# Kernel optimization log

Measured on AMD Instinct MI355X. Metric: run time of the kernel, lower is better.

## Reference

```python
import jax, jax.numpy as jnp
import numpy as np

K = 11
EPS = 1e-6


def _box_sum(a):
    # a: [B, H, W] -> KxK zero-padded local sum (equivalent to nn.Unfold padding=K//2 then sum)
    return jax.lax.reduce_window(a, 0.0, jax.lax.add,
                                 window_dimensions=(1, K, K),
                                 window_strides=(1, 1, 1),
                                 padding='SAME')


def setup_inputs() -> dict:
    key = jax.random.key(0)
    k1, k2 = jax.random.split(key)
    x = jax.random.normal(k1, (8, 3, 1024, 1024), dtype=jnp.float32)
    y = jax.random.normal(k2, (8, 3, 1024, 1024), dtype=jnp.float32)
    return {"x": x, "y": y}


def reference(x, y):
    # Channel-reduce first, then local KxK box sums (math-identical to the
    # unfold-based sum over (C, K, K) with zero padding).
    xx = _box_sum((x * x).sum(axis=1))   # [B, H, W]
    yy = _box_sum((y * y).sum(axis=1))
    xy = _box_sum((x * y).sum(axis=1))
    x_norm = jnp.sqrt(xx)
    y_norm = jnp.sqrt(yy)
    return xy / (x_norm * y_norm + EPS)
```

## Files before the change

### kernel.cpp

```cpp
#include <hip/hip_runtime.h>
#include <math.h>

#define NB 8
#define NC 3
#define NH 1024
#define NW 1024
#define EPS 1e-6f

#define BAND 128
#define CH 32
#define KSTEPS (CH + 10)
#define PADW 144

__global__ __launch_bounds__(64, 2)
void lcs_kernel(const float* __restrict__ x, const float* __restrict__ y,
                float* __restrict__ out) {
    __shared__ __align__(16) float P[2][3][PADW];

    const int l   = threadIdx.x;
    const int bid = blockIdx.x;
    const int b     = bid >> 8;
    const int rem   = bid & 255;
    const int band0 = (rem & 7) * BAND;
    const int r0    = (rem >> 3) * CH;

    const size_t chan = (size_t)NH * NW;
    const float* xb = x + (size_t)b * NC * chan;
    const float* yb = y + (size_t)b * NC * chan;

    const int gc0 = band0 - 8 + 2 * l;
    const int gcE = band0 + 120 + 2 * l;
    const float mm = (gc0 >= 0) ? 1.f : 0.f;
    const float me = (l < 8 && gcE + 1 <= NW - 1) ? 1.f : 0.f;
    const int o0 = (gc0 >= 0) ? gc0 : 0;
    const int oE = (me > 0.f) ? gcE : 0;

    float2 cur[12], nx1[12], nx2[12];
    auto ldrow = [&](int gr, float2* d) {
        const int rc = gr < 0 ? 0 : (gr > NH - 1 ? NH - 1 : gr);
        const size_t ro = (size_t)rc * NW;
        #pragma unroll
        for (int c = 0; c < 3; ++c) {
            const float* xr = xb + c * chan + ro;
            const float* yr = yb + c * chan + ro;
            d[c]     = *(const float2*)(xr + o0);
            d[3 + c] = *(const float2*)(yr + o0);
            d[6 + c] = *(const float2*)(xr + oE);
            d[9 + c] = *(const float2*)(yr + oE);
        }
    };

    ldrow(r0 - 5, cur);
    ldrow(r0 - 4, nx1);

    float2 ring[3][11];
    #pragma unroll
    for (int p = 0; p < 3; ++p)
        #pragma unroll
        for (int s = 0; s < 11; ++s) ring[p][s] = make_float2(0.f, 0.f);
    float2 vs[3] = {make_float2(0.f,0.f), make_float2(0.f,0.f), make_float2(0.f,0.f)};

    for (int g = 0; g < 4; ++g) {
        const int gg = g & 1;
        #pragma unroll
        for (int s = 0; s < 11; ++s) {
            const int k = g * 11 + s;
            if (k >= KSTEPS) continue;

            if (k + 2 < KSTEPS) ldrow(r0 - 3 + k, nx2);

            float2 pxx = make_float2(0.f,0.f), pyy = pxx, pxy = pxx;
            float2 qxx = pxx, qyy = pxx, qxy = pxx;
            #pragma unroll
            for (int c = 0; c < 3; ++c) {
                const float2 xm = cur[c],   ym = cur[3+c];
                const float2 xe = cur[6+c], ye = cur[9+c];
                pxx.x += xm.x*xm.x; pxx.y += xm.y*xm.y;
                pyy.x += ym.x*ym.x; pyy.y += ym.y*ym.y;
                pxy.x += xm.x*ym.x; pxy.y += xm.y*ym.y;
                qxx.x += xe.x*xe.x; qxx.y += xe.y*xe.y;
                qyy.x += ye.x*ye.x; qyy.y += ye.y*ye.y;
                qxy.x += xe.x*ye.x; qxy.y += xe.y*ye.y;
            }
            const int gr = r0 - 5 + k;
            const float rmf = (gr >= 0 && gr < NH) ? 1.f : 0.f;
            const float cmM = rmf * mm, cmE = rmf * me;
            pxx.x *= cmM; pxx.y *= cmM; pyy.x *= cmM; pyy.y *= cmM;
            pxy.x *= cmM; pxy.y *= cmM;
            qxx.x *= cmE; qxx.y *= cmE; qyy.x *= cmE; qyy.y *= cmE;
            qxy.x *= cmE; qxy.y *= cmE;

            const int pp = gg ^ (s & 1);
            float* Pb = &P[pp][0][0];

            ((float2*)(Pb + 0*PADW))[l] = pxx;
            ((float2*)(Pb + 1*PADW))[l] = pyy;
            ((float2*)(Pb + 2*PADW))[l] = pxy;
            if (l < 8) {
                ((float2*)(Pb + 0*PADW))[64 + l] = qxx;
                ((float2*)(Pb + 1*PADW))[64 + l] = qyy;
                ((float2*)(Pb + 2*PADW))[64 + l] = qxy;
            }
            __builtin_amdgcn_wave_barrier();

            #pragma unroll
            for (int p = 0; p < 3; ++p) {
                const float* Pq = Pb + p * PADW;
                float2 t[7];
                #pragma unroll
                for (int j = 0; j < 7; ++j)
                    t[j] = *(const float2*)(Pq + 2*l + 2 + 2*j);
                float h0 = ((t[0].y + t[1].x) + (t[1].y + t[2].x))
                         + ((t[2].y + t[3].x) + (t[3].y + t[4].x))
                         + ((t[4].y + t[5].x) + t[5].y);
                float h1 = h0 - t[0].y + t[6].x;
                vs[p].x += h0 - ring[p][s].x;
                vs[p].y += h1 - ring[p][s].y;
                ring[p][s].x = h0;
                ring[p][s].y = h1;
            }

            if (k >= 10) {
                const int orow = r0 + k - 10;
                const float d0 = __builtin_amdgcn_sqrtf(vs[0].x) *
                                 __builtin_amdgcn_sqrtf(vs[1].x) + EPS;
                const float d1 = __builtin_amdgcn_sqrtf(vs[0].y) *
                                 __builtin_amdgcn_sqrtf(vs[1].y) + EPS;
                float2 o;
                o.x = vs[2].x * __builtin_amdgcn_rcpf(d0);
                o.y = vs[2].y * __builtin_amdgcn_rcpf(d1);
                *(float2*)(out + ((size_t)b * NH + orow) * NW + band0 + 2*l) = o;
            }

            if (k + 1 < KSTEPS) {
                #pragma unroll
                for (int i = 0; i < 12; ++i) { cur[i] = nx1[i]; nx1[i] = nx2[i]; }
            }
        }
    }
}

extern "C" void kernel_launch(void* const* d_in, const int* in_sizes, int n_in,
                              void* d_out, int out_size, void* d_ws, size_t ws_size,
                              hipStream_t stream) {
    const float* x = (const float*)d_in[0];
    const float* y = (const float*)d_in[1];
    float* out = (float*)d_out;
    lcs_kernel<<<dim3(2048), dim3(64), 0, stream>>>(x, y, out);
}
```

Before: 241.3 us.

## Stream input rows into LDS via global_load_lds triple buffer

Replaces the register-held triple-buffered row prefetch with direct global-to-LDS loads (16-byte per lane) into a rotating three-slot LDS buffer, synchronized with explicit s_waitcnt vmcnt counts. Each lane loads one contiguous 16-byte segment per channel instead of two scattered float2 loads, and compute reads rows back from LDS. This cuts VGPR pressure and register shuffling and coalesces loads, but adds LDS usage and relies on hand-tuned vmcnt accounting; the LDS read after the wait lacks a barrier, and edge-column clamping changes the loaded layout, which risks correctness at the boundaries.

```diff
diff --git a/kernel.cpp b/kernel.cpp
--- a/kernel.cpp
+++ b/kernel.cpp
@@ -11,10 +11,15 @@
 #define CH 32
 #define KSTEPS (CH + 10)
 #define PADW 144
+#define SEGF 256
+
+typedef __attribute__((address_space(1))) const void gas_t;
+typedef __attribute__((address_space(3))) void las_t;
 
 __global__ __launch_bounds__(64, 2)
 void lcs_kernel(const float* __restrict__ x, const float* __restrict__ y,
                 float* __restrict__ out) {
+    __shared__ __align__(16) float R[3][6][SEGF];
     __shared__ __align__(16) float P[2][3][PADW];
 
     const int l   = threadIdx.x;
@@ -28,30 +33,34 @@
     const float* xb = x + (size_t)b * NC * chan;
     const float* yb = y + (size_t)b * NC * chan;
 
+    int oc = band0 - 8 + 4 * l;
+    oc = oc < 0 ? 0 : (oc > NW - 4 ? NW - 4 : oc);
+
     const int gc0 = band0 - 8 + 2 * l;
     const int gcE = band0 + 120 + 2 * l;
     const float mm = (gc0 >= 0) ? 1.f : 0.f;
     const float me = (l < 8 && gcE + 1 <= NW - 1) ? 1.f : 0.f;
-    const int o0 = (gc0 >= 0) ? gc0 : 0;
-    const int oE = (me > 0.f) ? gcE : 0;
+    const int eo = 2 * (l & 7);
 
-    float2 cur[12], nx1[12], nx2[12];
-    auto ldrow = [&](int gr, float2* d) {
+    auto dma_row = [&](int gr, float* slot) {
         const int rc = gr < 0 ? 0 : (gr > NH - 1 ? NH - 1 : gr);
         const size_t ro = (size_t)rc * NW;
         #pragma unroll
         for (int c = 0; c < 3; ++c) {
-            const float* xr = xb + c * chan + ro;
-            const float* yr = yb + c * chan + ro;
-            d[c]     = *(const float2*)(xr + o0);
-            d[3 + c] = *(const float2*)(yr + o0);
-            d[6 + c] = *(const float2*)(xr + oE);
-            d[9 + c] = *(const float2*)(yr + oE);
+            const float* gx = xb + c * chan + ro + oc;
+            const float* gy = yb + c * chan + ro + oc;
+            __builtin_amdgcn_global_load_lds((gas_t*)(const void*)gx,
+                                             (las_t*)(void*)(slot + c * SEGF), 16, 0, 0);
+            __builtin_amdgcn_global_load_lds((gas_t*)(const void*)gy,
+                                             (las_t*)(void*)(slot + (3 + c) * SEGF), 16, 0, 0);
         }
     };
 
-    ldrow(r0 - 5, cur);
-    ldrow(r0 - 4, nx1);
+    float* p0 = &R[0][0][0];
+    float* p1 = &R[1][0][0];
+    float* p2 = &R[2][0][0];
+    dma_row(r0 - 5, p0);
+    dma_row(r0 - 4, p1);
 
     float2 ring[3][11];
     #pragma unroll
@@ -67,14 +76,25 @@
             const int k = g * 11 + s;
             if (k >= KSTEPS) continue;
 
-            if (k + 2 < KSTEPS) ldrow(r0 - 3 + k, nx2);
+            if (k + 2 < KSTEPS) {
+                dma_row(r0 - 3 + k, p2);
+                asm volatile("s_waitcnt vmcnt(12)" ::: "memory");
+            } else {
+                asm volatile("s_waitcnt vmcnt(0)" ::: "memory");
+            }
+
+            const int gr = r0 - 5 + k;
+            const float rmf = (gr >= 0 && gr < NH) ? 1.f : 0.f;
+            const float cmM = rmf * mm, cmE = rmf * me;
 
             float2 pxx = make_float2(0.f,0.f), pyy = pxx, pxy = pxx;
             float2 qxx = pxx, qyy = pxx, qxy = pxx;
             #pragma unroll
             for (int c = 0; c < 3; ++c) {
-                const float2 xm = cur[c],   ym = cur[3+c];
-                const float2 xe = cur[6+c], ye = cur[9+c];
+                const float2 xm = *(const float2*)(p0 + c * SEGF + 2 * l);
+                const float2 ym = *(const float2*)(p0 + (3 + c) * SEGF + 2 * l);
+                const float2 xe = *(const float2*)(p0 + c * SEGF + 128 + eo);
+                const float2 ye = *(const float2*)(p0 + (3 + c) * SEGF + 128 + eo);
                 pxx.x += xm.x*xm.x; pxx.y += xm.y*xm.y;
                 pyy.x += ym.x*ym.x; pyy.y += ym.y*ym.y;
                 pxy.x += xm.x*ym.x; pxy.y += xm.y*ym.y;
@@ -82,9 +102,6 @@
                 qyy.x += ye.x*ye.x; qyy.y += ye.y*ye.y;
                 qxy.x += xe.x*ye.x; qxy.y += xe.y*ye.y;
             }
-            const int gr = r0 - 5 + k;
-            const float rmf = (gr >= 0 && gr < NH) ? 1.f : 0.f;
-            const float cmM = rmf * mm, cmE = rmf * me;
             pxx.x *= cmM; pxx.y *= cmM; pyy.x *= cmM; pyy.y *= cmM;
             pxy.x *= cmM; pxy.y *= cmM;
             qxx.x *= cmE; qxx.y *= cmE; qyy.x *= cmE; qyy.y *= cmE;
@@ -132,10 +149,7 @@
                 *(float2*)(out + ((size_t)b * NH + orow) * NW + band0 + 2*l) = o;
             }
 
-            if (k + 1 < KSTEPS) {
-                #pragma unroll
-                for (int i = 0; i < 12; ++i) { cur[i] = nx1[i]; nx1[i] = nx2[i]; }
-            }
+            float* tp = p0; p0 = p1; p1 = p2; p2 = tp;
         }
     }
 }
```

Result: slower. 277.5 us (+15.0%).
